# Kernel optimization log

Hardware: AMD Instinct MI355X
Metric: run time of the kernel (lower is better)

## Reference

```python
import jax, jax.numpy as jnp
import numpy as np

T_STEPS = 4
K = 16
TAU = 2.0      # spikingjelly LIFNode default tau
VTH = 1.0      # default v_threshold, v_reset=0, hard reset, decay_input=True
EPS = 1e-5
ALPHA = 2.0    # ATan surrogate default

@jax.custom_vjp
def spike(x):
    return (x >= 0.0).astype(x.dtype)

def _spike_fwd(x):
    return spike(x), x

def _spike_bwd(x, g):
    return (g * (ALPHA / 2.0) / (1.0 + (jnp.pi / 2.0 * ALPHA * x) ** 2),)

spike.defvjp(_spike_fwd, _spike_bwd)

def lif(x_seq):
    # multi-step LIF over leading time axis, v0=0
    def step(v, x):
        v = v + (x - v) / TAU          # decay_input=True, v_reset=0
        s = spike(v - VTH)
        return v * (1.0 - s), s        # hard reset to 0
    _, s_seq = jax.lax.scan(step, jnp.zeros_like(x_seq[0]), x_seq)
    return s_seq

def bntt(x, gamma, beta):
    # per-timestep BatchNorm (training-mode batch stats), x: [T,B,C,...]
    red = (1,) + tuple(range(3, x.ndim))
    mean = x.mean(axis=red, keepdims=True)
    var = ((x - mean) ** 2).mean(axis=red, keepdims=True)
    shp = (x.shape[0], 1, x.shape[2]) + (1,) * (x.ndim - 3)
    return (x - mean) * jax.lax.rsqrt(var + EPS) * gamma.reshape(shp) + beta.reshape(shp)

def graph_feature(x, k):
    # x: [B,C,N]; kNN on first 3 channels, DGCNN edge features [B,2C,N,k]
    pos = x[:, :3]
    inner = jnp.einsum('bcn,bcm->bnm', pos, pos)
    sq = jnp.sum(pos ** 2, axis=1)                     # [B,N]
    neg_d = 2.0 * inner - sq[:, :, None] - sq[:, None, :]
    idx = jax.lax.top_k(neg_d, k)[1]                   # [B,N,k]
    xt = jnp.swapaxes(x, 1, 2)                         # [B,N,C]
    nbr = jax.vmap(lambda f, i: f[i])(xt, idx)         # [B,N,k,C]
    ctr = xt[:, :, None, :]
    feat = jnp.concatenate([jnp.broadcast_to(ctr, nbr.shape), nbr - ctr], axis=-1)
    return jnp.transpose(feat, (0, 3, 1, 2))           # [B,2C,N,k]

def _forward(x, t_w1, t_b1, t_w2, t_b2, t_w3, t_b3, t_fw1, t_fb1, t_fw2, t_fb2,
             t_fw3, t_fb3, w1, w2, w3, w4, g1, be1, g2, be2, g3, be3, g4, be4):
    pos = x[:, :3]                                       # [B,3,N]
    # --- SpikingTNet ---
    xs = jnp.broadcast_to(pos[None], (T_STEPS,) + pos.shape)
    h = lif(jnp.einsum('tbcn,dc->tbdn', xs, t_w1) + t_b1[:, None])
    h = lif(jnp.einsum('tbcn,dc->tbdn', h, t_w2) + t_b2[:, None])
    h = lif(jnp.einsum('tbcn,dc->tbdn', h, t_w3) + t_b3[:, None])
    h = h.max(axis=3)                                    # [T,B,1024]
    h = lif(h @ t_fw1.T + t_fb1)
    h = lif(h @ t_fw2.T + t_fb2)
    h = h @ t_fw3.T + t_fb3                              # [T,B,9]
    trans = h.mean(axis=0).reshape(-1, 3, 3) + jnp.eye(3, dtype=x.dtype)
    # --- align + graph feature ---
    pos_a = jnp.einsum('bcn,bcd->bdn', pos, trans)
    xa = jnp.concatenate([pos_a, x[:, 3:]], axis=1)      # [B,14,N]
    gfeat = graph_feature(xa, K)                         # [B,28,N,K]
    gs = jnp.broadcast_to(gfeat[None], (T_STEPS,) + gfeat.shape)
    # --- spiking encoder ---
    h = lif(bntt(jnp.einsum('tbcnk,dc->tbdnk', gs, w1), g1, be1))
    h = lif(bntt(jnp.einsum('tbcnk,dc->tbdnk', h, w2), g2, be2))
    h = h.max(axis=4)                                    # [T,B,128,N]
    h = lif(bntt(jnp.einsum('tbcn,dc->tbdn', h, w3), g3, be3))
    h = lif(bntt(jnp.einsum('tbcn,dc->tbdn', h, w4), g4, be4))
    return h.max(axis=3).mean(axis=0)                    # [B,1024]

def setup_inputs():
    key = jax.random.key(0)
    ks = jax.random.split(key, 16)
    def w(i, shape, fan):
        return jax.random.normal(ks[i], shape, dtype=jnp.float32) / np.sqrt(fan)
    B, N = 8, 2048
    z = lambda *s: jnp.zeros(s, jnp.float32)
    o = lambda *s: jnp.ones(s, jnp.float32)
    return {
        'x': jax.random.normal(ks[0], (B, 14, N), dtype=jnp.float32),
        't_w1': w(1, (64, 3), 3), 't_b1': z(64),
        't_w2': w(2, (128, 64), 64), 't_b2': z(128),
        't_w3': w(3, (1024, 128), 128), 't_b3': z(1024),
        't_fw1': w(4, (512, 1024), 1024), 't_fb1': z(512),
        't_fw2': w(5, (256, 512), 512), 't_fb2': z(256),
        't_fw3': w(6, (9, 256), 256), 't_fb3': z(9),
        'w1': w(7, (64, 28), 28),
        'w2': w(8, (128, 64), 64),
        'w3': w(9, (256, 128), 128),
        'w4': w(10, (1024, 256), 256),
        'g1': o(T_STEPS, 64), 'be1': z(T_STEPS, 64),
        'g2': o(T_STEPS, 128), 'be2': z(T_STEPS, 128),
        'g3': o(T_STEPS, 256), 'be3': z(T_STEPS, 256),
        'g4': o(T_STEPS, 1024), 'be4': z(T_STEPS, 1024),
    }

def reference(x, t_w1, t_b1, t_w2, t_b2, t_w3, t_b3, t_fw1, t_fb1, t_fw2, t_fb2,
              t_fw3, t_fb3, w1, w2, w3, w4, g1, be1, g2, be2, g3, be3, g4, be4):
    return _forward(x, t_w1, t_b1, t_w2, t_b2, t_w3, t_b3, t_fw1, t_fb1, t_fw2,
                    t_fb2, t_fw3, t_fb3, w1, w2, w3, w4, g1, be1, g2, be2, g3,
                    be3, g4, be4)
```

## Files before the change

### kernel.cpp

```cpp
#include <hip/hip_runtime.h>
#include <stdint.h>

#define TT 4
#define BB 8
#define NN 2048
#define KNB 16
#define PP (NN*KNB)
#define VTH 1.0f
#define EPSB 1e-5f

typedef unsigned long long u64;
typedef unsigned int u32;
typedef unsigned short u16;
typedef unsigned char u8;
typedef __attribute__((ext_vector_type(8))) short short8;
typedef __attribute__((ext_vector_type(4))) float f4;

#define GLOAD_LDS16(g, l) __builtin_amdgcn_global_load_lds( \
    (const __attribute__((address_space(1))) u32*)(g), \
    (__attribute__((address_space(3))) u32*)(l), 16, 0, 0)

__device__ __forceinline__ float lif_step(float& v, float x) {
    v = v + (x - v) / 2.0f;
    float s = (v - VTH >= 0.0f) ? 1.0f : 0.0f;
    v = v * (1.0f - s);
    return s;
}

__global__ __launch_bounds__(256) void k_tnet1(const float* __restrict__ x, const float* __restrict__ w,
        const float* __restrict__ bi, u64* __restrict__ s1b) {
    int i = blockIdx.x*256 + threadIdx.x;
    int b = i >> 11, n = i & 2047;
    float p0 = x[((size_t)b*14+0)*NN+n];
    float p1 = x[((size_t)b*14+1)*NN+n];
    float p2 = x[((size_t)b*14+2)*NN+n];
    u64 m[TT] = {0,0,0,0};
    for (int d = 0; d < 64; ++d) {
        float z = ((w[d*3+0]*p0 + w[d*3+1]*p1) + w[d*3+2]*p2) + bi[d];
        float v = 0.f;
        #pragma unroll
        for (int t = 0; t < TT; ++t) {
            float s = lif_step(v, z);
            if (s != 0.f) m[t] |= (1ull << d);
        }
    }
    #pragma unroll
    for (int t = 0; t < TT; ++t) s1b[((size_t)t*BB + b)*NN + n] = m[t];
}

__global__ __launch_bounds__(256) void k_tnet2(const u64* __restrict__ s1b, const float* __restrict__ w,
        const float* __restrict__ bi, u32* __restrict__ s2b32) {
    __shared__ float ws[32*64];
    int tid = threadIdx.x;
    int ec = blockIdx.y;
    for (int l = tid; l < 32*64; l += 256) ws[l] = w[ec*32*64 + l];
    __syncthreads();
    int i = blockIdx.x*256 + tid;
    int b = i >> 11, n = i & 2047;
    u64 m[TT];
    #pragma unroll
    for (int t = 0; t < TT; ++t) m[t] = s1b[((size_t)t*BB+b)*NN+n];
    u32 o[TT] = {0,0,0,0};
    for (int el = 0; el < 32; ++el) {
        float z[TT] = {0.f,0.f,0.f,0.f};
        #pragma unroll 8
        for (int d = 0; d < 64; ++d) {
            float wv = ws[el*64+d];
            #pragma unroll
            for (int t = 0; t < TT; ++t) z[t] += ((m[t]>>d)&1ull) ? wv : 0.f;
        }
        float v = 0.f, bb = bi[ec*32 + el];
        #pragma unroll
        for (int t = 0; t < TT; ++t) {
            float s = lif_step(v, z[t] + bb);
            if (s != 0.f) o[t] |= (1u << el);
        }
    }
    #pragma unroll
    for (int t = 0; t < TT; ++t)
        s2b32[(((size_t)t*BB+b)*NN+n)*4 + ec] = o[t];
}

__global__ __launch_bounds__(512) void k_fc(const u32* __restrict__ mx, const float* __restrict__ fw1, const float* __restrict__ fb1,
        const float* __restrict__ fw2, const float* __restrict__ fb2, const float* __restrict__ fw3, const float* __restrict__ fb3,
        float* __restrict__ trans) {
    __shared__ float h0[TT][1024];
    __shared__ float h1[TT][512];
    __shared__ float h2[TT][256];
    __shared__ float h3s[TT][9];
    int b = blockIdx.x, tid = threadIdx.x;
    for (int l = tid; l < TT*1024; l += 512) h0[l>>10][l&1023] = (float)mx[((size_t)(l>>10)*BB + b)*1024 + (l&1023)];
    __syncthreads();
    {
        float z[TT] = {0.f,0.f,0.f,0.f};
        #pragma unroll 4
        for (int f = 0; f < 1024; ++f) {
            float wv = fw1[(size_t)tid*1024 + f];
            #pragma unroll
            for (int t = 0; t < TT; ++t) z[t] += wv * h0[t][f];
        }
        float v = 0.f;
        #pragma unroll
        for (int t = 0; t < TT; ++t) h1[t][tid] = lif_step(v, z[t] + fb1[tid]);
    }
    __syncthreads();
    if (tid < 256) {
        float z[TT] = {0.f,0.f,0.f,0.f};
        #pragma unroll 4
        for (int f = 0; f < 512; ++f) {
            float wv = fw2[(size_t)tid*512 + f];
            #pragma unroll
            for (int t = 0; t < TT; ++t) z[t] += wv * h1[t][f];
        }
        float v = 0.f;
        #pragma unroll
        for (int t = 0; t < TT; ++t) h2[t][tid] = lif_step(v, z[t] + fb2[tid]);
    }
    __syncthreads();
    if (tid < TT*9) {
        int t = tid/9, oo = tid%9;
        float z = 0.f;
        for (int f = 0; f < 256; ++f) z += fw3[oo*256+f]*h2[t][f];
        h3s[t][oo] = z + fb3[oo];
    }
    __syncthreads();
    if (tid < 9) {
        float m = ((h3s[0][tid]+h3s[1][tid]) + (h3s[2][tid]+h3s[3][tid])) * 0.25f;
        int c = tid/3, dd = tid%3;
        trans[b*9+tid] = m + ((c==dd)?1.0f:0.0f);
    }
}

__global__ __launch_bounds__(256) void k_trans(const float* __restrict__ x, const float* __restrict__ tr,
        float* __restrict__ xa, float4* __restrict__ xa4) {
    int i = blockIdx.x*256 + threadIdx.x;
    int b = i >> 11, n = i & 2047;
    float p0 = x[((size_t)b*14+0)*NN+n];
    float p1 = x[((size_t)b*14+1)*NN+n];
    float p2 = x[((size_t)b*14+2)*NN+n];
    const float* tb = tr + b*9;
    float a0 = (p0*tb[0] + p1*tb[3]) + p2*tb[6];
    float a1 = (p0*tb[1] + p1*tb[4]) + p2*tb[7];
    float a2 = (p0*tb[2] + p1*tb[5]) + p2*tb[8];
    xa[((size_t)b*14+0)*NN+n] = a0;
    xa[((size_t)b*14+1)*NN+n] = a1;
    xa[((size_t)b*14+2)*NN+n] = a2;
    for (int c = 3; c < 14; ++c) xa[((size_t)b*14+c)*NN+n] = x[((size_t)b*14+c)*NN+n];
    float4 p;
    p.x = a0; p.y = a1; p.z = a2;
    p.w = (a0*a0 + a1*a1) + a2*a2;
    xa4[(size_t)b*NN+n] = p;
}

__global__ __launch_bounds__(256) void k_knn(const float4* __restrict__ xa4, int* __restrict__ idx) {
    int wave = threadIdx.x >> 6, lane = threadIdx.x & 63;
    int b = blockIdx.y;
    int n = blockIdx.x*4 + wave;
    const float4* P = xa4 + (size_t)b*NN;
    float4 q = P[n];
    float sn = q.w;
    float vals[32];
    #pragma unroll
    for (int j = 0; j < 32; ++j) {
        float4 p = P[j*64 + lane];
        float inner = (q.x*p.x + q.y*p.y) + q.z*p.z;
        vals[j] = (2.0f*inner - sn) - p.w;
    }
    for (int k = 0; k < KNB; ++k) {
        float bv = -3.4e38f; int bj = 0;
        #pragma unroll
        for (int j = 0; j < 32; ++j) if (vals[j] > bv) { bv = vals[j]; bj = j; }
        int bm = bj*64 + lane;
        u32 fb = __float_as_uint(bv);
        fb = (fb & 0x80000000u) ? ~fb : (fb | 0x80000000u);
        u64 key = ((u64)fb << 32) | (u32)(~bm);
        #pragma unroll
        for (int o2 = 1; o2 < 64; o2 <<= 1) {
            u64 other = __shfl_xor(key, o2, 64);
            key = (other > key) ? other : key;
        }
        int wm = (int)(~(u32)key);
        if (lane == 0) idx[((size_t)b*NN + n)*KNB + k] = wm;
        int wl = wm & 63, wj = wm >> 6;
        if (lane == wl) {
            #pragma unroll
            for (int j = 0; j < 32; ++j) if (j == wj) vals[j] = -3.4e38f;
        }
    }
}

__global__ __launch_bounds__(256) void k_gfeat(const float* __restrict__ xa, const int* __restrict__ idx, float* __restrict__ gf) {
    int i = blockIdx.x*256 + threadIdx.x;
    int b = i >> 15;
    int r = i & 32767;
    int n = r >> 4;
    int mm = idx[((size_t)b*NN+n)*KNB + (r & 15)];
    size_t pbase = (size_t)b*28*PP + r;
    #pragma unroll
    for (int c = 0; c < 14; ++c) {
        float ctr = xa[((size_t)b*14+c)*NN + n];
        float nb  = xa[((size_t)b*14+c)*NN + mm];
        gf[pbase + (size_t)c*PP] = ctr;
        gf[pbase + (size_t)(14+c)*PP] = nb - ctr;
    }
}

__global__ __launch_bounds__(256) void k_estats1(const float* __restrict__ gf, const float* __restrict__ w1, float* __restrict__ part1) {
    __shared__ float gfs[28][256];
    __shared__ float w1s[64*28];
    __shared__ float wsum[4][64], wsq[4][64];
    int pt = blockIdx.x, b = blockIdx.y;
    int p0 = pt*256, tid = threadIdx.x;
    for (int l = tid; l < 28*256; l += 256) gfs[l>>8][l&255] = gf[((size_t)b*28 + (l>>8))*PP + p0 + (l&255)];
    for (int l = tid; l < 64*28; l += 256) w1s[l] = w1[l];
    __syncthreads();
    int wv = tid>>6, lane = tid&63;
    for (int d = 0; d < 64; ++d) {
        float z = 0.f;
        #pragma unroll
        for (int c = 0; c < 28; ++c) z += w1s[d*28+c]*gfs[c][tid];
        float s = z, q = z*z;
        #pragma unroll
        for (int o = 1; o < 64; o <<= 1) { s += __shfl_xor(s, o, 64); q += __shfl_xor(q, o, 64); }
        if (lane == 0) { wsum[wv][d] = s; wsq[wv][d] = q; }
    }
    __syncthreads();
    if (tid < 64) {
        float s = (wsum[0][tid]+wsum[1][tid])+(wsum[2][tid]+wsum[3][tid]);
        float q = (wsq[0][tid]+wsq[1][tid])+(wsq[2][tid]+wsq[3][tid]);
        size_t blk = (size_t)b*128 + pt;
        part1[(blk*64 + tid)*2+0] = s;
        part1[(blk*64 + tid)*2+1] = q;
    }
}

__global__ __launch_bounds__(256) void k_reduce(const float* __restrict__ part, float* __restrict__ stats, int nch, int nblk, double M) {
    __shared__ double sred[256], qred[256];
    int ch = blockIdx.x, tid = threadIdx.x;
    double s = 0.0, q = 0.0;
    for (int i = tid; i < nblk; i += 256) {
        s += (double)part[((size_t)i*nch + ch)*2 + 0];
        q += (double)part[((size_t)i*nch + ch)*2 + 1];
    }
    sred[tid] = s; qred[tid] = q;
    __syncthreads();
    for (int off = 128; off > 0; off >>= 1) {
        if (tid < off) { sred[tid] += sred[tid+off]; qred[tid] += qred[tid+off]; }
        __syncthreads();
    }
    if (tid == 0) {
        double mu = sred[0] / M;
        double var = qred[0] / M - mu*mu;
        if (var < 0.0) var = 0.0;
        stats[ch*2+0] = (float)mu;
        stats[ch*2+1] = 1.0f / sqrtf((float)var + EPSB);
    }
}

__global__ __launch_bounds__(256) void k_h1(const float* __restrict__ gf, const float* __restrict__ w1,
        const float* __restrict__ st1, const float* __restrict__ g1, const float* __restrict__ be1,
        u64* __restrict__ h1b, u64* __restrict__ h1n) {
    __shared__ float w1s[64*28];
    int tid = threadIdx.x;
    int b = blockIdx.y;
    int p0 = blockIdx.x*256;
    int p = p0 + tid;
    for (int l = tid; l < 64*28; l += 256) w1s[l] = w1[l];
    __syncthreads();
    float gr[28];
    #pragma unroll
    for (int c = 0; c < 28; ++c) gr[c] = gf[((size_t)b*28 + c)*PP + p];
    int wordbase = (p0>>6) + (tid>>6);
    u64 pm[TT] = {0,0,0,0};
    for (int d = 0; d < 64; ++d) {
        float z = 0.f;
        #pragma unroll
        for (int c = 0; c < 28; ++c) z += w1s[d*28+c]*gr[c];
        float mu = st1[d*2+0], iv = st1[d*2+1];
        float v = 0.f;
        #pragma unroll
        for (int t = 0; t < TT; ++t) {
            float y = (z - mu) * iv * g1[t*64+d] + be1[t*64+d];
            float s = lif_step(v, y);
            u64 m = __ballot(s != 0.f);
            if ((tid & 63) == 0) h1b[((size_t)(t*BB+b)*64 + d)*512 + wordbase] = m;
            pm[t] |= ((u64)(s != 0.f)) << d;
        }
    }
    #pragma unroll
    for (int t = 0; t < TT; ++t) h1n[(size_t)(t*BB+b)*PP + p] = pm[t];
}

__global__ __launch_bounds__(256) void k_gram_h1(const u64* __restrict__ h1b, int* __restrict__ Mi) {
    __shared__ u64 tw[64*65];
    int tid = threadIdx.x;
    int w0 = blockIdx.x*64;
    int tb = blockIdx.y;
    int t = tb >> 3;
    const u64* src = h1b + (size_t)tb*64*512;
    for (int l = tid; l < 64*64; l += 256) {
        int c = l >> 6, w = l & 63;
        tw[c*65+w] = src[(size_t)c*512 + w0 + w];
    }
    __syncthreads();
    int q = tid >> 4, r = tid & 15;
    int acc[4][4];
    #pragma unroll
    for (int i=0;i<4;++i)
        #pragma unroll
        for (int j=0;j<4;++j) acc[i][j]=0;
    #pragma unroll 4
    for (int w = 0; w < 64; ++w) {
        u64 av[4], bv[4];
        #pragma unroll
        for (int i=0;i<4;++i) av[i] = tw[(q+16*i)*65+w];
        #pragma unroll
        for (int j=0;j<4;++j) bv[j] = tw[(r+16*j)*65+w];
        #pragma unroll
        for (int i=0;i<4;++i)
            #pragma unroll
            for (int j=0;j<4;++j) acc[i][j] += (int)__popcll(av[i]&bv[j]);
    }
    #pragma unroll
    for (int i=0;i<4;++i)
        #pragma unroll
        for (int j=0;j<4;++j)
            atomicAdd(&Mi[((size_t)t*64 + q+16*i)*64 + r+16*j], acc[i][j]);
}

template<int C>
__global__ __launch_bounds__(256) void k_gram2(const u64* __restrict__ bits, int* __restrict__ Mi) {
    __shared__ u64 ta[64*33], tbt[64*33];
    int tid = threadIdx.x;
    int ci0 = blockIdx.x*64, cj0 = blockIdx.y*64;
    int tb = blockIdx.z;
    int t = tb >> 3;
    const u64* srcA = bits + ((size_t)tb*C + ci0)*32;
    const u64* srcB = bits + ((size_t)tb*C + cj0)*32;
    for (int l = tid; l < 64*32; l += 256) {
        int rr = l >> 5, w = l & 31;
        ta[rr*33+w]  = srcA[(size_t)rr*32+w];
        tbt[rr*33+w] = srcB[(size_t)rr*32+w];
    }
    __syncthreads();
    int q = tid >> 4, r = tid & 15;
    int acc[4][4];
    #pragma unroll
    for (int i=0;i<4;++i)
        #pragma unroll
        for (int j=0;j<4;++j) acc[i][j]=0;
    #pragma unroll 4
    for (int w = 0; w < 32; ++w) {
        u64 av[4], bv[4];
        #pragma unroll
        for (int i=0;i<4;++i) av[i] = ta[(q+16*i)*33+w];
        #pragma unroll
        for (int j=0;j<4;++j) bv[j] = tbt[(r+16*j)*33+w];
        #pragma unroll
        for (int i=0;i<4;++i)
            #pragma unroll
            for (int j=0;j<4;++j) acc[i][j] += (int)__popcll(av[i]&bv[j]);
    }
    #pragma unroll
    for (int i=0;i<4;++i)
        #pragma unroll
        for (int j=0;j<4;++j)
            atomicAdd(&Mi[((size_t)t*C + ci0+q+16*i)*C + cj0+r+16*j], acc[i][j]);
}

template<int CIN>
__global__ void k_proj(const int* __restrict__ Mf, const float* __restrict__ w,
        float* __restrict__ st, int COUT, double cnt) {
    __shared__ double z2s[256], mns[256];
    int ch = blockIdx.x, t = blockIdx.y, c2 = threadIdx.x;
    const int* Mt = Mf + (size_t)t*CIN*CIN;
    double y = 0.0;
    for (int c = 0; c < CIN; ++c)
        y += (double)w[(size_t)ch*CIN+c] * (double)Mt[(size_t)c*CIN + c2];
    double wc2 = (double)w[(size_t)ch*CIN+c2];
    z2s[c2] = wc2 * y;
    mns[c2] = wc2 * (double)Mt[(size_t)c2*CIN + c2];
    __syncthreads();
    for (int off = CIN>>1; off > 0; off >>= 1) {
        if (c2 < off) { z2s[c2] += z2s[c2+off]; mns[c2] += mns[c2+off]; }
        __syncthreads();
    }
    if (c2 == 0) {
        double mu = mns[0] / cnt;
        double var = z2s[0] / cnt - mu*mu;
        if (var < 0.0) var = 0.0;
        st[((size_t)t*COUT+ch)*2+0] = (float)mu;
        st[((size_t)t*COUT+ch)*2+1] = 1.0f / sqrtf((float)var + EPSB);
    }
}

__global__ __launch_bounds__(256) void k_wprep(const float* __restrict__ w,
        short* __restrict__ hi, short* __restrict__ mid, short* __restrict__ lo, int F, int K) {
    int i = blockIdx.x*256 + threadIdx.x;
    if (i >= F*K) return;
    int f = i / K, k = i % K;
    float wv = w[i];
    u32 b0 = __float_as_uint(wv);
    float h = __uint_as_float(b0 & 0xFFFF0000u);
    float r1 = wv - h;
    u32 b1 = __float_as_uint(r1);
    float m = __uint_as_float(b1 & 0xFFFF0000u);
    float r2 = r1 - m;
    u32 b2 = __float_as_uint(r2);
    size_t o = ((size_t)(k>>3)*F + f)*8 + (k&7);
    hi[o]  = (short)(b0 >> 16);
    mid[o] = (short)(b1 >> 16);
    lo[o]  = (short)(b2 >> 16);
}

template<int K, int F, int MODE, bool BITS>
__global__ __launch_bounds__(256) void k_mconv(
        const void* __restrict__ Asrc,
        const short* __restrict__ Whi, const short* __restrict__ Wmd, const short* __restrict__ Wlo,
        const float* __restrict__ st, const float* __restrict__ ga, const float* __restrict__ be,
        const float* __restrict__ bias,
        u16* __restrict__ outp, u32* __restrict__ outm, int NPTS) {
    constexpr int KT = (K < 128) ? K : 128;
    constexpr int ROWS = (KT/8)*3;
    __shared__ short wsm[(KT/8)*3*512];
    __shared__ u32 morr[TT][64];
    int tid = threadIdx.x;
    int wave = tid >> 6, lane = tid & 63;
    int l15 = lane & 15, lg = lane >> 4;
    int b = blockIdx.z;
    int n_base = blockIdx.x*64 + wave*16;
    int f0 = blockIdx.y*64;
    if (MODE == 0 || MODE == 2)
        for (int l = tid; l < TT*64; l += 256) morr[l>>6][l&63] = 0u;

    f4 acc[4][TT];
    #pragma unroll
    for (int i = 0; i < 4; ++i)
        #pragma unroll
        for (int t = 0; t < TT; ++t) acc[i][t] = (f4)0.f;

    const u64* Ab[TT];
    const u16* Au[TT];
    #pragma unroll
    for (int t = 0; t < TT; ++t) {
        if (BITS) Ab[t] = (const u64*)Asrc + ((size_t)(t*BB+b)*NPTS + n_base + l15)*(K/64);
        else      Au[t] = (const u16*)Asrc + ((size_t)(t*BB+b)*NPTS + n_base + l15)*K + lg*8;
    }
    const short* Wsrc[3] = {Whi, Wmd, Wlo};

    for (int kt = 0; kt < K; kt += KT) {
        if (kt > 0) __syncthreads();
        for (int r = wave; r < ROWS; r += 4) {
            int kq = r/3, s = r - kq*3;
            const short* g = Wsrc[s] + ((size_t)((kt>>3) + kq)*F + f0)*8 + lane*8;
            GLOAD_LDS16(g, &wsm[r*512]);
        }
        __syncthreads();
        for (int k0 = 0; k0 < KT; k0 += 32) {
            int kg = kt + k0;
            short8 a[TT];
            #pragma unroll
            for (int t = 0; t < TT; ++t) {
                if (BITS) {
                    int kk = kg + lg*8;
                    u64 word = Ab[t][kk >> 6];
                    u32 byte = (u32)(word >> (kk & 63)) & 0xFFu;
                    #pragma unroll
                    for (int j = 0; j < 8; ++j) a[t][j] = (short)(((byte>>j)&1u) * 0x3F80u);
                } else {
                    a[t] = *(const short8*)(Au[t] + kg);
                }
            }
            int kql = (k0>>3) + lg;
            #pragma unroll
            for (int fs = 0; fs < 4; ++fs) {
                const short* base = wsm + kql*1536 + (fs*16+l15)*8;
                short8 whi = *(const short8*)(base);
                short8 wmd = *(const short8*)(base + 512);
                short8 wlo = *(const short8*)(base + 1024);
                #pragma unroll
                for (int t = 0; t < TT; ++t) {
                    acc[fs][t] = __builtin_amdgcn_mfma_f32_16x16x32_bf16(a[t], whi, acc[fs][t], 0, 0, 0);
                    acc[fs][t] = __builtin_amdgcn_mfma_f32_16x16x32_bf16(a[t], wmd, acc[fs][t], 0, 0, 0);
                    acc[fs][t] = __builtin_amdgcn_mfma_f32_16x16x32_bf16(a[t], wlo, acc[fs][t], 0, 0, 0);
                }
            }
        }
    }
    if (MODE == 1) {
        #pragma unroll
        for (int fs = 0; fs < 4; ++fs) {
            int f = f0 + fs*16 + l15;
            #pragma unroll
            for (int reg = 0; reg < 4; ++reg) {
                int n = n_base + lg*4 + reg;
                float v = 0.f;
                #pragma unroll
                for (int t = 0; t < TT; ++t) {
                    int ch = t*F + f;
                    float y = (acc[fs][t][reg] - st[(size_t)ch*2+0])*st[(size_t)ch*2+1]*ga[ch] + be[ch];
                    float s = lif_step(v, y);
                    outp[((size_t)(t*BB+b)*NPTS + n)*F + f] = (s != 0.f) ? (u16)0x3F80 : (u16)0;
                }
            }
        }
    } else if (MODE == 3) {
        #pragma unroll
        for (int fs = 0; fs < 4; ++fs) {
            int f = f0 + fs*16 + l15;
            u32 nib = 0u;
            #pragma unroll
            for (int reg = 0; reg < 4; ++reg) {
                float v = 0.f;
                #pragma unroll
                for (int t = 0; t < TT; ++t) {
                    int ch = t*F + f;
                    float y = (acc[fs][t][reg] - st[(size_t)ch*2+0])*st[(size_t)ch*2+1]*ga[ch] + be[ch];
                    float s = lif_step(v, y);
                    if (s != 0.f) nib |= (1u << t);
                }
            }
            nib |= __shfl_xor(nib, 16, 64);
            nib |= __shfl_xor(nib, 32, 64);
            if (lg == 0) {
                int n_pt = n_base >> 4;
                #pragma unroll
                for (int t = 0; t < TT; ++t)
                    outp[((size_t)(t*BB+b)*(NPTS>>4) + n_pt)*F + f] = ((nib>>t)&1u) ? (u16)0x3F80 : (u16)0;
            }
        }
    } else {
        #pragma unroll
        for (int fs = 0; fs < 4; ++fs) {
            int f = f0 + fs*16 + l15;
            u32 any[TT] = {0,0,0,0};
            float bb = (MODE == 0) ? bias[f] : 0.f;
            #pragma unroll
            for (int reg = 0; reg < 4; ++reg) {
                float v = 0.f;
                #pragma unroll
                for (int t = 0; t < TT; ++t) {
                    float y;
                    if (MODE == 0) y = acc[fs][t][reg] + bb;
                    else {
                        int ch = t*F + f;
                        y = (acc[fs][t][reg] - st[(size_t)ch*2+0])*st[(size_t)ch*2+1]*ga[ch] + be[ch];
                    }
                    float s = lif_step(v, y);
                    if (s != 0.f) any[t] = 1u;
                }
            }
            #pragma unroll
            for (int t = 0; t < TT; ++t) if (any[t]) atomicOr(&morr[t][fs*16+l15], 1u);
        }
        __syncthreads();
        for (int l = tid; l < TT*64; l += 256)
            if (morr[l>>6][l&63]) atomicOr(&outm[((size_t)((l>>6)*BB+b))*F + f0 + (l&63)], 1u);
    }
}

template<int C>
__global__ __launch_bounds__(256) void k_repack(const u16* __restrict__ sp, u64* __restrict__ bits) {
    __shared__ u16 tile[64][C+2];
    int tid = threadIdx.x;
    int nw = blockIdx.x, b = blockIdx.y, t = blockIdx.z;
    const u16* src = sp + ((size_t)(t*BB+b)*NN + nw*64)*C;
    for (int i = tid*2; i < 64*C; i += 512) {
        u32 v = *(const u32*)(src + i);
        int r = i / C, c = i % C;
        *(u32*)&tile[r][c] = v;
    }
    __syncthreads();
    int wave = tid >> 6, lane = tid & 63;
    for (int c = wave; c < C; c += 4) {
        u64 m = __ballot(tile[lane][c] != 0);
        if (lane == 0) bits[((size_t)(t*BB+b)*C + c)*32 + nw] = m;
    }
}

__global__ __launch_bounds__(256) void k_out(const u32* __restrict__ mx4, float* __restrict__ out) {
    int i = blockIdx.x*256 + threadIdx.x;
    int b = i >> 10, g = i & 1023;
    float s = (float)(mx4[((size_t)0*BB+b)*1024+g] + mx4[((size_t)1*BB+b)*1024+g]
                    + mx4[((size_t)2*BB+b)*1024+g] + mx4[((size_t)3*BB+b)*1024+g]);
    out[i] = s * 0.25f;
}

extern "C" void kernel_launch(void* const* d_in, const int* in_sizes, int n_in,
                              void* d_out, int out_size, void* d_ws, size_t ws_size,
                              hipStream_t stream) {
    (void)in_sizes; (void)n_in; (void)out_size;
    const float* x    = (const float*)d_in[0];
    const float* tw1  = (const float*)d_in[1];
    const float* tb1  = (const float*)d_in[2];
    const float* tw2  = (const float*)d_in[3];
    const float* tb2  = (const float*)d_in[4];
    const float* tw3  = (const float*)d_in[5];
    const float* tb3  = (const float*)d_in[6];
    const float* tfw1 = (const float*)d_in[7];
    const float* tfb1 = (const float*)d_in[8];
    const float* tfw2 = (const float*)d_in[9];
    const float* tfb2 = (const float*)d_in[10];
    const float* tfw3 = (const float*)d_in[11];
    const float* tfb3 = (const float*)d_in[12];
    const float* w1   = (const float*)d_in[13];
    const float* w2   = (const float*)d_in[14];
    const float* w3   = (const float*)d_in[15];
    const float* w4   = (const float*)d_in[16];
    const float* g1   = (const float*)d_in[17];
    const float* be1  = (const float*)d_in[18];
    const float* g2   = (const float*)d_in[19];
    const float* be2  = (const float*)d_in[20];
    const float* g3   = (const float*)d_in[21];
    const float* be3  = (const float*)d_in[22];
    const float* g4   = (const float*)d_in[23];
    const float* be4  = (const float*)d_in[24];

    char* wsb = (char*)d_ws;
    size_t off = 0;
    auto alloc = [&](size_t bytes) -> void* {
        void* p = wsb + off;
        off = (off + bytes + 255) & ~(size_t)255;
        return p;
    };
    u64* s1b   = (u64*)alloc(sizeof(u64)*(size_t)TT*BB*NN);
    u64* s2b   = (u64*)alloc(sizeof(u64)*(size_t)TT*BB*NN*2);
    u32* mx    = (u32*)alloc(sizeof(u32)*(size_t)TT*BB*1024);
    u32* mx4   = (u32*)alloc(sizeof(u32)*(size_t)TT*BB*1024);
    float* trs = (float*)alloc(sizeof(float)*BB*9);
    float* xa  = (float*)alloc(sizeof(float)*(size_t)BB*14*NN);
    float4* xa4 = (float4*)alloc(sizeof(float4)*(size_t)BB*NN);
    int* idx   = (int*)alloc(sizeof(int)*(size_t)BB*NN*KNB);
    float* gf  = (float*)alloc(sizeof(float)*(size_t)BB*28*PP);
    float* part1 = (float*)alloc(sizeof(float)*(size_t)1024*64*2);
    float* st1 = (float*)alloc(sizeof(float)*64*2);
    float* st2 = (float*)alloc(sizeof(float)*512*2);
    float* st3 = (float*)alloc(sizeof(float)*1024*2);
    float* st4 = (float*)alloc(sizeof(float)*4096*2);
    u64* h1b = (u64*)alloc(sizeof(u64)*(size_t)TT*BB*64*512);
    u64* h1n = (u64*)alloc(sizeof(u64)*(size_t)TT*BB*PP);
    u16* m2p = (u16*)alloc(sizeof(u16)*(size_t)TT*BB*NN*128);
    u16* h3p = (u16*)alloc(sizeof(u16)*(size_t)TT*BB*NN*256);
    u64* m2b = (u64*)alloc(sizeof(u64)*(size_t)TT*BB*128*32);
    u64* h3b = (u64*)alloc(sizeof(u64)*(size_t)TT*BB*256*32);
    int* Mi64  = (int*)alloc(sizeof(int)*(size_t)TT*64*64);
    int* Mi128 = (int*)alloc(sizeof(int)*(size_t)TT*128*128);
    int* Mi256 = (int*)alloc(sizeof(int)*(size_t)TT*256*256);
    short* wp2h = (short*)alloc(sizeof(short)*(size_t)128*64);
    short* wp2m = (short*)alloc(sizeof(short)*(size_t)128*64);
    short* wp2l = (short*)alloc(sizeof(short)*(size_t)128*64);
    short* wp3h = (short*)alloc(sizeof(short)*(size_t)256*128);
    short* wp3m = (short*)alloc(sizeof(short)*(size_t)256*128);
    short* wp3l = (short*)alloc(sizeof(short)*(size_t)256*128);
    short* wp4h = (short*)alloc(sizeof(short)*(size_t)1024*256);
    short* wp4m = (short*)alloc(sizeof(short)*(size_t)1024*256);
    short* wp4l = (short*)alloc(sizeof(short)*(size_t)1024*256);
    short* wpth = (short*)alloc(sizeof(short)*(size_t)1024*128);
    short* wptm = (short*)alloc(sizeof(short)*(size_t)1024*128);
    short* wptl = (short*)alloc(sizeof(short)*(size_t)1024*128);
    if (off > ws_size) return;

    hipMemsetAsync(mx, 0, sizeof(u32)*(size_t)TT*BB*1024, stream);
    hipMemsetAsync(mx4, 0, sizeof(u32)*(size_t)TT*BB*1024, stream);
    hipMemsetAsync(Mi64, 0, sizeof(int)*(size_t)TT*64*64, stream);
    hipMemsetAsync(Mi128, 0, sizeof(int)*(size_t)TT*128*128, stream);
    hipMemsetAsync(Mi256, 0, sizeof(int)*(size_t)TT*256*256, stream);

    k_wprep<<<dim3((128*64+255)/256), dim3(256), 0, stream>>>(w2, wp2h, wp2m, wp2l, 128, 64);
    k_wprep<<<dim3((256*128+255)/256), dim3(256), 0, stream>>>(w3, wp3h, wp3m, wp3l, 256, 128);
    k_wprep<<<dim3((1024*256+255)/256), dim3(256), 0, stream>>>(w4, wp4h, wp4m, wp4l, 1024, 256);
    k_wprep<<<dim3((1024*128+255)/256), dim3(256), 0, stream>>>(tw3, wpth, wptm, wptl, 1024, 128);

    k_tnet1<<<dim3(64), dim3(256), 0, stream>>>(x, tw1, tb1, s1b);
    k_tnet2<<<dim3(64, 4), dim3(256), 0, stream>>>(s1b, tw2, tb2, (u32*)s2b);
    k_mconv<128,1024,0,true><<<dim3(32,16,8), dim3(256), 0, stream>>>(
        s2b, wpth, wptm, wptl, nullptr, nullptr, nullptr, tb3, nullptr, mx, NN);
    k_fc<<<dim3(8), dim3(512), 0, stream>>>(mx, tfw1, tfb1, tfw2, tfb2, tfw3, tfb3, trs);
    k_trans<<<dim3(64), dim3(256), 0, stream>>>(x, trs, xa, xa4);
    k_knn<<<dim3(NN/4, BB), dim3(256), 0, stream>>>(xa4, idx);
    k_gfeat<<<dim3((BB*NN*KNB)/256), dim3(256), 0, stream>>>(xa, idx, gf);
    k_estats1<<<dim3(128, 8), dim3(256), 0, stream>>>(gf, w1, part1);
    k_reduce<<<dim3(64), dim3(256), 0, stream>>>(part1, st1, 64, 1024, 262144.0);
    k_h1<<<dim3(128, 8), dim3(256), 0, stream>>>(gf, w1, st1, g1, be1, h1b, h1n);
    k_gram_h1<<<dim3(8, TT*BB), dim3(256), 0, stream>>>(h1b, Mi64);
    k_proj<64><<<dim3(128, TT), dim3(64), 0, stream>>>(Mi64, w2, st2, 128, 262144.0);
    k_mconv<64,128,3,true><<<dim3(PP/64,2,8), dim3(256), 0, stream>>>(
        h1n, wp2h, wp2m, wp2l, st2, g2, be2, nullptr, m2p, nullptr, PP);
    k_repack<128><<<dim3(32,8,4), dim3(256), 0, stream>>>(m2p, m2b);
    k_gram2<128><<<dim3(2,2,TT*BB), dim3(256), 0, stream>>>(m2b, Mi128);
    k_proj<128><<<dim3(256, TT), dim3(128), 0, stream>>>(Mi128, w3, st3, 256, 16384.0);
    k_mconv<128,256,1,false><<<dim3(32,4,8), dim3(256), 0, stream>>>(
        m2p, wp3h, wp3m, wp3l, st3, g3, be3, nullptr, h3p, nullptr, NN);
    k_repack<256><<<dim3(32,8,4), dim3(256), 0, stream>>>(h3p, h3b);
    k_gram2<256><<<dim3(4,4,TT*BB), dim3(256), 0, stream>>>(h3b, Mi256);
    k_proj<256><<<dim3(1024, TT), dim3(256), 0, stream>>>(Mi256, w4, st4, 1024, 16384.0);
    k_mconv<256,1024,2,false><<<dim3(32,16,8), dim3(256), 0, stream>>>(
        h3p, wp4h, wp4m, wp4l, st4, g4, be4, nullptr, nullptr, mx4, NN);
    k_out<<<dim3(32), dim3(256), 0, stream>>>(mx4, (float*)d_out);
}
```

Measured before the change: 822.6 us.

## Split TNet FC head across many blocks and speed bit-unpacking in mconv

The single 8-block FC head kernel is split into three kernels: fc1 and fc2 now run one wavefront per output feature and batch, with coalesced weight reads and shuffle reductions. This spreads work that was serialized over very few blocks across the whole GPU. In k_mconv the K tile is fixed at 64, the packed spike words are preloaded into registers, and the bit-to-bf16 expansion uses an LDS lookup table instead of per-bit arithmetic. It adds two kernel launches, small intermediate buffers, and LDS lookups that could cause bank conflicts.

```diff
diff --git a/kernel.cpp b/kernel.cpp
--- a/kernel.cpp
+++ b/kernel.cpp
@@ -81,46 +81,64 @@
         s2b32[(((size_t)t*BB+b)*NN+n)*4 + ec] = o[t];
 }
 
-__global__ __launch_bounds__(512) void k_fc(const u32* __restrict__ mx, const float* __restrict__ fw1, const float* __restrict__ fb1,
-        const float* __restrict__ fw2, const float* __restrict__ fb2, const float* __restrict__ fw3, const float* __restrict__ fb3,
-        float* __restrict__ trans) {
-    __shared__ float h0[TT][1024];
-    __shared__ float h1[TT][512];
-    __shared__ float h2[TT][256];
+__global__ __launch_bounds__(64) void k_fc1(const u32* __restrict__ mx, const float* __restrict__ fw1,
+        const float* __restrict__ fb1, float* __restrict__ h1v) {
+    int f = blockIdx.x, b = blockIdx.y, lane = threadIdx.x;
+    float wr[16];
+    #pragma unroll
+    for (int j = 0; j < 16; ++j) wr[j] = fw1[(size_t)f*1024 + j*64 + lane];
+    float z[TT];
+    #pragma unroll
+    for (int t = 0; t < TT; ++t) {
+        float s = 0.f;
+        #pragma unroll
+        for (int j = 0; j < 16; ++j)
+            s += wr[j] * (float)mx[((size_t)t*BB+b)*1024 + j*64 + lane];
+        #pragma unroll
+        for (int o = 1; o < 64; o <<= 1) s += __shfl_xor(s, o, 64);
+        z[t] = s;
+    }
+    if (lane == 0) {
+        float v = 0.f;
+        #pragma unroll
+        for (int t = 0; t < TT; ++t)
+            h1v[((size_t)t*BB+b)*512 + f] = lif_step(v, z[t] + fb1[f]);
+    }
+}
+
+__global__ __launch_bounds__(64) void k_fc2(const float* __restrict__ h1v, const float* __restrict__ fw2,
+        const float* __restrict__ fb2, float* __restrict__ h2v) {
+    int f = blockIdx.x, b = blockIdx.y, lane = threadIdx.x;
+    float wr[8];
+    #pragma unroll
+    for (int j = 0; j < 8; ++j) wr[j] = fw2[(size_t)f*512 + j*64 + lane];
+    float z[TT];
+    #pragma unroll
+    for (int t = 0; t < TT; ++t) {
+        float s = 0.f;
+        #pragma unroll
+        for (int j = 0; j < 8; ++j)
+            s += wr[j] * h1v[((size_t)t*BB+b)*512 + j*64 + lane];
+        #pragma unroll
+        for (int o = 1; o < 64; o <<= 1) s += __shfl_xor(s, o, 64);
+        z[t] = s;
+    }
+    if (lane == 0) {
+        float v = 0.f;
+        #pragma unroll
+        for (int t = 0; t < TT; ++t)
+            h2v[((size_t)t*BB+b)*256 + f] = lif_step(v, z[t] + fb2[f]);
+    }
+}
+
+__global__ __launch_bounds__(64) void k_fc3(const float* __restrict__ h2v, const float* __restrict__ fw3,
+        const float* __restrict__ fb3, float* __restrict__ trans) {
     __shared__ float h3s[TT][9];
     int b = blockIdx.x, tid = threadIdx.x;
-    for (int l = tid; l < TT*1024; l += 512) h0[l>>10][l&1023] = (float)mx[((size_t)(l>>10)*BB + b)*1024 + (l&1023)];
-    __syncthreads();
-    {
-        float z[TT] = {0.f,0.f,0.f,0.f};
-        #pragma unroll 4
-        for (int f = 0; f < 1024; ++f) {
-            float wv = fw1[(size_t)tid*1024 + f];
-            #pragma unroll
-            for (int t = 0; t < TT; ++t) z[t] += wv * h0[t][f];
-        }
-        float v = 0.f;
-        #pragma unroll
-        for (int t = 0; t < TT; ++t) h1[t][tid] = lif_step(v, z[t] + fb1[tid]);
-    }
-    __syncthreads();
-    if (tid < 256) {
-        float z[TT] = {0.f,0.f,0.f,0.f};
-        #pragma unroll 4
-        for (int f = 0; f < 512; ++f) {
-            float wv = fw2[(size_t)tid*512 + f];
-            #pragma unroll
-            for (int t = 0; t < TT; ++t) z[t] += wv * h1[t][f];
-        }
-        float v = 0.f;
-        #pragma unroll
-        for (int t = 0; t < TT; ++t) h2[t][tid] = lif_step(v, z[t] + fb2[tid]);
-    }
-    __syncthreads();
     if (tid < TT*9) {
         int t = tid/9, oo = tid%9;
         float z = 0.f;
-        for (int f = 0; f < 256; ++f) z += fw3[oo*256+f]*h2[t][f];
+        for (int c = 0; c < 256; ++c) z += fw3[oo*256+c]*h2v[((size_t)t*BB+b)*256 + c];
         h3s[t][oo] = z + fb3[oo];
     }
     __syncthreads();
@@ -420,9 +438,11 @@
         const float* __restrict__ st, const float* __restrict__ ga, const float* __restrict__ be,
         const float* __restrict__ bias,
         u16* __restrict__ outp, u32* __restrict__ outm, int NPTS) {
-    constexpr int KT = (K < 128) ? K : 128;
+    constexpr int KT = 64;
     constexpr int ROWS = (KT/8)*3;
-    __shared__ short wsm[(KT/8)*3*512];
+    constexpr int NW = (K+63)/64;
+    __shared__ short wsm[ROWS*512];
+    __shared__ short sptab[BITS ? 256*8 : 8];
     __shared__ u32 morr[TT][64];
     int tid = threadIdx.x;
     int wave = tid >> 6, lane = tid & 63;
@@ -432,6 +452,10 @@
     int f0 = blockIdx.y*64;
     if (MODE == 0 || MODE == 2)
         for (int l = tid; l < TT*64; l += 256) morr[l>>6][l&63] = 0u;
+    if (BITS) {
+        #pragma unroll
+        for (int j = 0; j < 8; ++j) sptab[tid*8+j] = (short)(((tid>>j)&1) * 0x3F80);
+    }
 
     f4 acc[4][TT];
     #pragma unroll
@@ -439,34 +463,39 @@
         #pragma unroll
         for (int t = 0; t < TT; ++t) acc[i][t] = (f4)0.f;
 
-    const u64* Ab[TT];
+    u64 aw[TT][NW];
     const u16* Au[TT];
     #pragma unroll
     for (int t = 0; t < TT; ++t) {
-        if (BITS) Ab[t] = (const u64*)Asrc + ((size_t)(t*BB+b)*NPTS + n_base + l15)*(K/64);
-        else      Au[t] = (const u16*)Asrc + ((size_t)(t*BB+b)*NPTS + n_base + l15)*K + lg*8;
+        if (BITS) {
+            const u64* Ab = (const u64*)Asrc + ((size_t)(t*BB+b)*NPTS + n_base + l15)*NW;
+            #pragma unroll
+            for (int wq = 0; wq < NW; ++wq) aw[t][wq] = Ab[wq];
+        } else {
+            Au[t] = (const u16*)Asrc + ((size_t)(t*BB+b)*NPTS + n_base + l15)*K + lg*8;
+        }
     }
     const short* Wsrc[3] = {Whi, Wmd, Wlo};
 
+    #pragma unroll
     for (int kt = 0; kt < K; kt += KT) {
         if (kt > 0) __syncthreads();
+        #pragma unroll
         for (int r = wave; r < ROWS; r += 4) {
             int kq = r/3, s = r - kq*3;
             const short* g = Wsrc[s] + ((size_t)((kt>>3) + kq)*F + f0)*8 + lane*8;
             GLOAD_LDS16(g, &wsm[r*512]);
         }
         __syncthreads();
+        #pragma unroll
         for (int k0 = 0; k0 < KT; k0 += 32) {
             int kg = kt + k0;
             short8 a[TT];
             #pragma unroll
             for (int t = 0; t < TT; ++t) {
                 if (BITS) {
-                    int kk = kg + lg*8;
-                    u64 word = Ab[t][kk >> 6];
-                    u32 byte = (u32)(word >> (kk & 63)) & 0xFFu;
-                    #pragma unroll
-                    for (int j = 0; j < 8; ++j) a[t][j] = (short)(((byte>>j)&1u) * 0x3F80u);
+                    u32 byte = (u32)(aw[t][kg>>6] >> ((kg&63) + lg*8)) & 0xFFu;
+                    a[t] = *(const short8*)(sptab + byte*8);
                 } else {
                     a[t] = *(const short8*)(Au[t] + kg);
                 }
@@ -637,6 +666,8 @@
     float* st2 = (float*)alloc(sizeof(float)*512*2);
     float* st3 = (float*)alloc(sizeof(float)*1024*2);
     float* st4 = (float*)alloc(sizeof(float)*4096*2);
+    float* h1v = (float*)alloc(sizeof(float)*(size_t)TT*BB*512);
+    float* h2v = (float*)alloc(sizeof(float)*(size_t)TT*BB*256);
     u64* h1b = (u64*)alloc(sizeof(u64)*(size_t)TT*BB*64*512);
     u64* h1n = (u64*)alloc(sizeof(u64)*(size_t)TT*BB*PP);
     u16* m2p = (u16*)alloc(sizeof(u16)*(size_t)TT*BB*NN*128);
@@ -675,7 +706,9 @@
     k_tnet2<<<dim3(64, 4), dim3(256), 0, stream>>>(s1b, tw2, tb2, (u32*)s2b);
     k_mconv<128,1024,0,true><<<dim3(32,16,8), dim3(256), 0, stream>>>(
         s2b, wpth, wptm, wptl, nullptr, nullptr, nullptr, tb3, nullptr, mx, NN);
-    k_fc<<<dim3(8), dim3(512), 0, stream>>>(mx, tfw1, tfb1, tfw2, tfb2, tfw3, tfb3, trs);
+    k_fc1<<<dim3(512, 8), dim3(64), 0, stream>>>(mx, tfw1, tfb1, h1v);
+    k_fc2<<<dim3(256, 8), dim3(64), 0, stream>>>(h1v, tfw2, tfb2, h2v);
+    k_fc3<<<dim3(8), dim3(64), 0, stream>>>(h2v, tfw3, tfb3, trs);
     k_trans<<<dim3(64), dim3(256), 0, stream>>>(x, trs, xa, xa4);
     k_knn<<<dim3(NN/4, BB), dim3(256), 0, stream>>>(xa4, idx);
     k_gfeat<<<dim3((BB*NN*KNB)/256), dim3(256), 0, stream>>>(xa, idx, gf);
```

Result: faster. 730.7 us (-11.2%).
